# Kernel optimization log

Measured on AMD Instinct MI355X. Metric: run time of the kernel, lower is better.

The kernel has to match this reference:

```python
import jax, jax.numpy as jnp
import numpy as np


def setup_inputs() -> dict:
    T, B, D = 2048, 16, 1024
    key = jax.random.key(0)
    ks = jax.random.split(key, 6)
    scale = 1.0 / np.sqrt(D)  # keep matmul outputs O(1) like xavier/orthogonal init
    return {
        "x": jax.random.normal(ks[0], (T, B, D), dtype=jnp.float32),
        "h0": jnp.zeros((B, D), dtype=jnp.float32),
        "W_alpha": jax.random.normal(ks[1], (D, D), dtype=jnp.float32) * scale,
        "b_alpha": jnp.full((D,), 2.0, dtype=jnp.float32),
        "W_beta": jax.random.normal(ks[2], (D, D), dtype=jnp.float32) * scale,
        "b_beta": jnp.zeros((D,), dtype=jnp.float32),
        "W_h": jax.random.normal(ks[3], (D, D), dtype=jnp.float32) * (0.5 * scale),
        "W_x": jax.random.normal(ks[4], (D, D), dtype=jnp.float32) * scale,
        "b": jnp.zeros((D,), dtype=jnp.float32),
    }


def reference(x, h0, W_alpha, b_alpha, W_beta, b_beta, W_h, W_x, b):
    # x: (T, B, D). Precompute all input-dependent projections as one big GEMM each.
    alpha_all = jax.nn.sigmoid(jnp.einsum("tbd,ed->tbe", x, W_alpha) + b_alpha)  # (T,B,D)
    beta_all = jax.nn.sigmoid(jnp.einsum("tbd,ed->tbe", x, W_beta) + b_beta)
    Wx_all = jnp.einsum("tbd,ed->tbe", x, W_x) + b

    def step(h_prev, inp):
        alpha, beta, wx = inp
        v = jnp.tanh(h_prev @ W_h.T + wx)
        h_new = alpha * h_prev + beta * v
        out = h_new * jax.nn.silu(h_new)
        return h_new, (h_new, out)

    _, (h_seq, output) = jax.lax.scan(step, h0, (alpha_all, beta_all, Wx_all))
    h = jnp.concatenate([h0[None], h_seq], axis=0)  # (T+1, B, D)
    return output, h
```

## Files before the change

### kernel.cpp

```cpp
#include <hip/hip_runtime.h>
#include <stdint.h>
#include <stddef.h>

static constexpr int  T_STEPS   = 2048;
static constexpr int  BATCH     = 16;
static constexpr int  DIM       = 1024;
static constexpr long RROWS     = (long)T_STEPS * BATCH;
static constexpr long BD        = (long)BATCH * DIM;
static constexpr long OUT_ELEMS = (long)T_STEPS * BD;

static constexpr size_t WX_OFF  = 0;
static constexpr size_t XBF_OFF = 134217728;
static constexpr size_t WHI_OFF = XBF_OFF + 67108864;
static constexpr size_t WLO_OFF = WHI_OFF + 6291456;
static constexpr size_t HBP_OFF = WLO_OFF + 6291456;

typedef __attribute__((ext_vector_type(2))) float          f32x2;
typedef __attribute__((ext_vector_type(4))) float          f32x4;
typedef __attribute__((ext_vector_type(8))) short          s16x8;
typedef __attribute__((ext_vector_type(4))) unsigned short u16x4;
typedef __attribute__((ext_vector_type(8))) unsigned short u16x8;

#define AS1 __attribute__((address_space(1)))
#define AS3 __attribute__((address_space(3)))

static __device__ __forceinline__ unsigned short f2bf(float x) {
  union { float f; unsigned u; } a; a.f = x;
  unsigned r = a.u + 0x7fffu + ((a.u >> 16) & 1u);
  return (unsigned short)(r >> 16);
}
static __device__ __forceinline__ float bf2f(unsigned short h) {
  union { unsigned u; float f; } a; a.u = ((unsigned)h) << 16; return a.f;
}
static __device__ __forceinline__ void gload_lds16(const void* g, void* l) {
  __builtin_amdgcn_global_load_lds((const AS1 void*)g, (AS3 void*)l, 16, 0, 0);
}
static __device__ __forceinline__ float fast_tanh(float z) {
  return 1.0f - 2.0f / (__expf(2.0f * z) + 1.0f);
}

__global__ __launch_bounds__(256) void convert_x_kernel(const float* __restrict__ x,
                                                        unsigned short* __restrict__ xbf) {
  const long n8 = (RROWS * DIM) / 8;
  const long stride = (long)gridDim.x * blockDim.x;
  for (long i = (long)blockIdx.x * blockDim.x + threadIdx.x; i < n8; i += stride) {
    const float4* p = (const float4*)(x + i * 8);
    float4 v0 = p[0], v1 = p[1];
    u16x8 o;
    o[0] = f2bf(v0.x); o[1] = f2bf(v0.y); o[2] = f2bf(v0.z); o[3] = f2bf(v0.w);
    o[4] = f2bf(v1.x); o[5] = f2bf(v1.y); o[6] = f2bf(v1.z); o[7] = f2bf(v1.w);
    *(u16x8*)(xbf + i * 8) = o;
  }
}

__global__ __launch_bounds__(256) void convert_w_kernel(const float* __restrict__ Wa,
                                                        const float* __restrict__ Wb,
                                                        const float* __restrict__ Wx,
                                                        unsigned short* __restrict__ whi,
                                                        unsigned short* __restrict__ wlo) {
  const long n4 = (3l * 1024 * 1024) / 4;
  const long stride = (long)gridDim.x * blockDim.x;
  for (long i = (long)blockIdx.x * blockDim.x + threadIdx.x; i < n4; i += stride) {
    long e = i * 4;
    int mat = (int)(e >> 20);
    long off = e & 1048575l;
    const float* src = (mat == 0) ? Wa : (mat == 1) ? Wb : Wx;
    float4 v = *(const float4*)(src + off);
    u16x4 hi, lo;
    hi[0] = f2bf(v.x); lo[0] = f2bf(v.x - bf2f(hi[0]));
    hi[1] = f2bf(v.y); lo[1] = f2bf(v.y - bf2f(hi[1]));
    hi[2] = f2bf(v.z); lo[2] = f2bf(v.z - bf2f(hi[2]));
    hi[3] = f2bf(v.w); lo[3] = f2bf(v.w - bf2f(hi[3]));
    *(u16x4*)(whi + e) = hi;
    *(u16x4*)(wlo + e) = lo;
  }
}

__global__ __launch_bounds__(256) void gemm_pre(
    const unsigned short* __restrict__ xbf,
    const unsigned short* __restrict__ whi,
    const unsigned short* __restrict__ wlo,
    const float* __restrict__ b_alpha, const float* __restrict__ b_beta, const float* __restrict__ b_x,
    float* __restrict__ alpha_dst, float* __restrict__ beta_dst, float* __restrict__ wx_dst)
{
  __shared__ unsigned short Al[128 * 64];
  __shared__ unsigned short Bh[128 * 64];
  __shared__ unsigned short Bl[128 * 64];
  const int tid  = threadIdx.x;
  const int lane = tid & 63;
  const int w    = tid >> 6;
  const int wm   = w >> 1, wn = w & 1;
  const long rowA0 = (long)blockIdx.x * 128;
  const int  colB0 = blockIdx.y * 128;

  f32x4 acc[4][4];
#pragma unroll
  for (int i = 0; i < 4; ++i)
#pragma unroll
    for (int j = 0; j < 4; ++j) acc[i][j] = (f32x4){0.f, 0.f, 0.f, 0.f};

  for (int k0 = 0; k0 < 1024; k0 += 64) {
#pragma unroll
    for (int is = 0; is < 4; ++is) {
      const int o   = is * 4096 + tid * 16;
      const int row = o >> 7;
      const int ke  = (o & 127) >> 1;
      const long asrc = (rowA0 + row) * 1024 + (k0 + ke);
      const long bsrc = ((long)(colB0 + row)) * 1024 + (k0 + ke);
      gload_lds16(xbf + asrc, (char*)Al + is * 4096 + w * 1024);
      gload_lds16(whi + bsrc, (char*)Bh + is * 4096 + w * 1024);
      gload_lds16(wlo + bsrc, (char*)Bl + is * 4096 + w * 1024);
    }
    asm volatile("s_waitcnt vmcnt(0)" ::: "memory");
    __syncthreads();
#pragma unroll
    for (int kk = 0; kk < 2; ++kk) {
      const int koff = kk * 64 + ((lane >> 4) * 16);
      s16x8 a[4], bhf[4], blf[4];
#pragma unroll
      for (int i = 0; i < 4; ++i)
        a[i] = *(const s16x8*)((const char*)Al + (wm * 64 + i * 16 + (lane & 15)) * 128 + koff);
#pragma unroll
      for (int j = 0; j < 4; ++j) {
        const int r = (wn * 64 + j * 16 + (lane & 15)) * 128 + koff;
        bhf[j] = *(const s16x8*)((const char*)Bh + r);
        blf[j] = *(const s16x8*)((const char*)Bl + r);
      }
#pragma unroll
      for (int i = 0; i < 4; ++i)
#pragma unroll
        for (int j = 0; j < 4; ++j) {
          acc[i][j] = __builtin_amdgcn_mfma_f32_16x16x32_bf16(a[i], bhf[j], acc[i][j], 0, 0, 0);
          acc[i][j] = __builtin_amdgcn_mfma_f32_16x16x32_bf16(a[i], blf[j], acc[i][j], 0, 0, 0);
        }
    }
    __syncthreads();
  }

  const int region = colB0 >> 10;
  const float* bias = (region == 0) ? b_alpha : (region == 1) ? b_beta : b_x;
  float* dst = (region == 0) ? alpha_dst : (region == 1) ? beta_dst : wx_dst;
#pragma unroll
  for (int j = 0; j < 4; ++j) {
    const int colg = colB0 + wn * 64 + j * 16 + (lane & 15);
    const int nl = colg & 1023;
    const float bj = bias[nl];
#pragma unroll
    for (int i = 0; i < 4; ++i) {
#pragma unroll
      for (int r = 0; r < 4; ++r) {
        const long rowg = rowA0 + wm * 64 + i * 16 + ((lane >> 4) * 4) + r;
        float z = acc[i][j][r] + bj;
        float val = (region == 2) ? z : (1.0f / (1.0f + __expf(-z)));
        dst[rowg * 1024 + nl] = val;
      }
    }
  }
}

__global__ __launch_bounds__(256, 1) void scan_kernel(
    const float* __restrict__ Wh,
    const float* __restrict__ h0,
    const float* __restrict__ wxb,
    float* __restrict__ out_buf,
    float* __restrict__ h_out,
    unsigned* __restrict__ hbp)
{
  __shared__ unsigned short WhiL[32 * 1024];
  __shared__ unsigned short WloL[32 * 1024];
  __shared__ __align__(16) float zred[2][4][16][34];

  const int tid  = threadIdx.x;
  const int lane = tid & 63;
  const int w    = tid >> 6;
  const int wg   = blockIdx.x;
  const int n0   = wg * 32;

  {
    const int row = tid >> 3;
    const int kb  = (tid & 7) * 128;
    const float* src = Wh + (size_t)(n0 + row) * 1024 + kb;
    const unsigned sx = ((unsigned)(row & 7)) << 4;
    const unsigned rb = (unsigned)row * 2048u;
#pragma unroll
    for (int q = 0; q < 32; ++q) {
      float4 v = *(const float4*)(src + q * 4);
      u16x4 hi, lo;
      hi[0] = f2bf(v.x); lo[0] = f2bf(v.x - bf2f(hi[0]));
      hi[1] = f2bf(v.y); lo[1] = f2bf(v.y - bf2f(hi[1]));
      hi[2] = f2bf(v.z); lo[2] = f2bf(v.z - bf2f(hi[2]));
      hi[3] = f2bf(v.w); lo[3] = f2bf(v.w - bf2f(hi[3]));
      const unsigned addr = (rb + (unsigned)(kb + q * 4) * 2u) ^ sx;
      *(u16x4*)((char*)WhiL + addr) = hi;
      *(u16x4*)((char*)WloL + addr) = lo;
    }
  }

  const int b_own = tid >> 4;
  const int nl    = tid & 15;
  const long off0 = (long)b_own * 1024 + n0 + 2 * nl;
  const int  pword = b_own * 512 + wg * 16 + nl;

  const int arow = lane & 15;
  const int gk   = lane >> 4;
  const unsigned bswz = ((unsigned)(arow & 7)) << 4;

  f32x2 hpv = *(const f32x2*)(h0 + off0);
  float hp0 = hpv[0], hp1 = hpv[1];
  *(f32x2*)(h_out + off0) = hpv;
  {
    unsigned pv = ((unsigned)f2bf(hp1) << 16) | (unsigned)(f2bf(hp0) & 0xFFFEu);
    __hip_atomic_store(hbp + pword, pv, __ATOMIC_RELAXED, __HIP_MEMORY_SCOPE_AGENT);
  }
  __syncthreads();

  f32x2 acv = *(const f32x2*)(h_out + BD + off0);
  f32x2 bcv = *(const f32x2*)(out_buf + off0);
  f32x2 wcv = *(const f32x2*)(wxb + off0);
  float a_c0 = acv[0], a_c1 = acv[1], b_c0 = bcv[0], b_c1 = bcv[1], w_c0 = wcv[0], w_c1 = wcv[1];

  float dh0 = 0.f, dh1 = 0.f;

  for (int t = 0; t < T_STEPS; ++t) {
    const unsigned eps = (unsigned)((t >> 1) & 1);
    const unsigned long long* base64 =
        (const unsigned long long*)hbp +
        (((size_t)(t & 1) * 8192 + (long)arow * 512 + w * 128 + gk * 4) >> 1);

    unsigned long long vv[8][2];
#pragma unroll
    for (int q = 0; q < 8; ++q) {
      vv[q][0] = __hip_atomic_load(base64 + q * 8,     __ATOMIC_RELAXED, __HIP_MEMORY_SCOPE_AGENT);
      vv[q][1] = __hip_atomic_load(base64 + q * 8 + 1, __ATOMIC_RELAXED, __HIP_MEMORY_SCOPE_AGENT);
    }

    float a_n0 = 0.f, a_n1 = 0.f, b_n0 = 0.f, b_n1 = 0.f, w_n0 = 0.f, w_n1 = 0.f;
    if (t + 1 < T_STEPS) {
      const long o = (long)(t + 1) * BD + off0;
      f32x2 an = __builtin_nontemporal_load((const f32x2*)(h_out + BD + o));
      f32x2 bn = __builtin_nontemporal_load((const f32x2*)(out_buf + o));
      f32x2 wn = __builtin_nontemporal_load((const f32x2*)(wxb + o));
      a_n0 = an[0]; a_n1 = an[1]; b_n0 = bn[0]; b_n1 = bn[1]; w_n0 = wn[0]; w_n1 = wn[1];
    }
    __builtin_amdgcn_sched_barrier(0);

    if (t > 0) {
      const long od = (long)(t - 1) * BD + off0;
      f32x2 hv; hv[0] = dh0; hv[1] = dh1;
      __builtin_nontemporal_store(hv, (f32x2*)(h_out + BD + od));
      const float sg0 = 1.0f / (1.0f + __expf(-dh0));
      const float sg1 = 1.0f / (1.0f + __expf(-dh1));
      f32x2 ov; ov[0] = dh0 * dh0 * sg0; ov[1] = dh1 * dh1 * sg1;
      __builtin_nontemporal_store(ov, (f32x2*)(out_buf + od));
    }

    f32x4 acc0 = (f32x4){0.f,0.f,0.f,0.f};
    f32x4 acc1 = (f32x4){0.f,0.f,0.f,0.f};
    const unsigned kbase = (unsigned)(w * 256 + gk * 8) * 2u;
    union Frag { unsigned long long u[2]; s16x8 h; };

#define DO_CHUNK(Q, V)                                                          \
    {                                                                           \
      Frag fh; fh.u[0] = (V)[0]; fh.u[1] = (V)[1];                              \
      const unsigned kb = kbase + (unsigned)(Q) * 64u;                          \
      const unsigned a0 = ((unsigned)arow * 2048u + kb) ^ bswz;                 \
      const unsigned a1 = ((unsigned)(16 + arow) * 2048u + kb) ^ bswz;          \
      s16x8 bh0 = *(const s16x8*)((const char*)WhiL + a0);                      \
      s16x8 bl0 = *(const s16x8*)((const char*)WloL + a0);                      \
      s16x8 bh1 = *(const s16x8*)((const char*)WhiL + a1);                      \
      s16x8 bl1 = *(const s16x8*)((const char*)WloL + a1);                      \
      acc0 = __builtin_amdgcn_mfma_f32_16x16x32_bf16(fh.h, bh0, acc0, 0, 0, 0); \
      acc0 = __builtin_amdgcn_mfma_f32_16x16x32_bf16(fh.h, bl0, acc0, 0, 0, 0); \
      acc1 = __builtin_amdgcn_mfma_f32_16x16x32_bf16(fh.h, bh1, acc1, 0, 0, 0); \
      acc1 = __builtin_amdgcn_mfma_f32_16x16x32_bf16(fh.h, bl1, acc1, 0, 0, 0); \
    }

    unsigned pend = 0;
#pragma unroll
    for (int q = 0; q < 8; ++q) {
      unsigned bad = 0;
#pragma unroll
      for (int d = 0; d < 2; ++d) {
        bad |= ((unsigned)vv[q][d] ^ eps) & 1u;
        bad |= ((unsigned)(vv[q][d] >> 32) ^ eps) & 1u;
      }
      if (__all(bad == 0u)) { DO_CHUNK(q, vv[q]); }
      else                  { pend |= 1u << q; }
    }

    int iters = 0;
    while (pend) {
#pragma unroll
      for (int q = 0; q < 8; ++q)
        if (pend & (1u << q)) {
          vv[q][0] = __hip_atomic_load(base64 + q * 8,     __ATOMIC_RELAXED, __HIP_MEMORY_SCOPE_AGENT);
          vv[q][1] = __hip_atomic_load(base64 + q * 8 + 1, __ATOMIC_RELAXED, __HIP_MEMORY_SCOPE_AGENT);
        }
      __builtin_amdgcn_sched_barrier(0);
#pragma unroll
      for (int q = 0; q < 8; ++q) {
        if (pend & (1u << q)) {
          unsigned bad = 0;
#pragma unroll
          for (int d = 0; d < 2; ++d) {
            bad |= ((unsigned)vv[q][d] ^ eps) & 1u;
            bad |= ((unsigned)(vv[q][d] >> 32) ^ eps) & 1u;
          }
          if (__all(bad == 0u)) { DO_CHUNK(q, vv[q]); pend &= ~(1u << q); }
        }
      }
      if (++iters > (1 << 15)) break;
    }
#undef DO_CHUNK

    const int tb = t & 1;
#pragma unroll
    for (int r = 0; r < 4; ++r) {
      zred[tb][w][gk * 4 + r][arow]      = acc0[r];
      zred[tb][w][gk * 4 + r][16 + arow] = acc1[r];
    }
    __syncthreads();

    float z0 = w_c0, z1 = w_c1;
#pragma unroll
    for (int wv = 0; wv < 4; ++wv) {
      f32x2 p = *(const f32x2*)&zred[tb][wv][b_own][2 * nl];
      z0 += p[0]; z1 += p[1];
    }
    const float v0 = fast_tanh(z0), v1 = fast_tanh(z1);
    const float hn0 = a_c0 * hp0 + b_c0 * v0;
    const float hn1 = a_c1 * hp1 + b_c1 * v1;

    if (t + 1 < T_STEPS) {
      const unsigned epn = (unsigned)(((t + 1) >> 1) & 1);
      unsigned pv = ((unsigned)f2bf(hn1) << 16)
                  | (unsigned)((f2bf(hn0) & 0xFFFEu) | epn);
      __hip_atomic_store(hbp + ((size_t)((t + 1) & 1) * 8192 + pword), pv,
                         __ATOMIC_RELAXED, __HIP_MEMORY_SCOPE_AGENT);
    }

    dh0 = hn0; dh1 = hn1;
    hp0 = hn0; hp1 = hn1;
    a_c0 = a_n0; a_c1 = a_n1; b_c0 = b_n0; b_c1 = b_n1; w_c0 = w_n0; w_c1 = w_n1;
  }

  {
    const long od = (long)(T_STEPS - 1) * BD + off0;
    f32x2 hv; hv[0] = dh0; hv[1] = dh1;
    __builtin_nontemporal_store(hv, (f32x2*)(h_out + BD + od));
    const float sg0 = 1.0f / (1.0f + __expf(-dh0));
    const float sg1 = 1.0f / (1.0f + __expf(-dh1));
    f32x2 ov; ov[0] = dh0 * dh0 * sg0; ov[1] = dh1 * dh1 * sg1;
    __builtin_nontemporal_store(ov, (f32x2*)(out_buf + od));
  }
}

extern "C" void kernel_launch(void* const* d_in, const int* in_sizes, int n_in,
                              void* d_out, int out_size, void* d_ws, size_t ws_size,
                              hipStream_t stream) {
  const float* x  = (const float*)d_in[0];
  const float* h0 = (const float*)d_in[1];
  const float* Wa = (const float*)d_in[2];
  const float* ba = (const float*)d_in[3];
  const float* Wb = (const float*)d_in[4];
  const float* bb = (const float*)d_in[5];
  const float* Wh = (const float*)d_in[6];
  const float* Wx = (const float*)d_in[7];
  const float* bx = (const float*)d_in[8];

  float* out_buf = (float*)d_out;
  float* h_out   = out_buf + OUT_ELEMS;

  char* ws = (char*)d_ws;
  float*          wx_buf = (float*)(ws + WX_OFF);
  unsigned short* xbf    = (unsigned short*)(ws + XBF_OFF);
  unsigned short* whi    = (unsigned short*)(ws + WHI_OFF);
  unsigned short* wlo    = (unsigned short*)(ws + WLO_OFF);
  unsigned*       hbp    = (unsigned*)(ws + HBP_OFF);

  hipMemsetAsync(hbp, 0xFF, 65536, stream);
  convert_x_kernel<<<4096, 256, 0, stream>>>(x, xbf);
  convert_w_kernel<<<1024, 256, 0, stream>>>(Wa, Wb, Wx, whi, wlo);
  gemm_pre<<<dim3(256, 24), 256, 0, stream>>>(xbf, whi, wlo, ba, bb, bx,
                                              h_out + BD, out_buf, wx_buf);
  scan_kernel<<<32, 256, 0, stream>>>(Wh, h0, wx_buf, out_buf, h_out, hbp);
}
```

Before: 8.220 ms.

## Run recurrent scan step on a single wavefront, removing LDS reduction and barrier

The per-step scan work in each block moves from four wavefronts that split K to a single wavefront that walks all 32 K-chunks itself, keeping two accumulator sets per output tile. This removes the per-step shared-memory partial-sum reduction and the __syncthreads between wavefronts, and the epilogue now writes bf16-packed h using lane shuffles. In exchange, one wavefront issues four times as many MFMAs and polling loads per step, with more registers held live and less latency hiding.

```diff
diff --git a/kernel.cpp b/kernel.cpp
--- a/kernel.cpp
+++ b/kernel.cpp
@@ -168,13 +168,10 @@
 {
   __shared__ unsigned short WhiL[32 * 1024];
   __shared__ unsigned short WloL[32 * 1024];
-  __shared__ __align__(16) float zred[2][4][16][34];
-
-  const int tid  = threadIdx.x;
-  const int lane = tid & 63;
-  const int w    = tid >> 6;
-  const int wg   = blockIdx.x;
-  const int n0   = wg * 32;
+
+  const int tid = threadIdx.x;
+  const int wg  = blockIdx.x;
+  const int n0  = wg * 32;
 
   {
     const int row = tid >> 3;
@@ -195,163 +192,202 @@
       *(u16x4*)((char*)WloL + addr) = lo;
     }
   }
-
-  const int b_own = tid >> 4;
-  const int nl    = tid & 15;
-  const long off0 = (long)b_own * 1024 + n0 + 2 * nl;
-  const int  pword = b_own * 512 + wg * 16 + nl;
-
+  __syncthreads();
+  if (tid >= 64) return;
+
+  const int lane = tid;
   const int arow = lane & 15;
   const int gk   = lane >> 4;
   const unsigned bswz = ((unsigned)(arow & 7)) << 4;
 
-  f32x2 hpv = *(const f32x2*)(h0 + off0);
-  float hp0 = hpv[0], hp1 = hpv[1];
-  *(f32x2*)(h_out + off0) = hpv;
-  {
-    unsigned pv = ((unsigned)f2bf(hp1) << 16) | (unsigned)(f2bf(hp0) & 0xFFFEu);
-    __hip_atomic_store(hbp + pword, pv, __ATOMIC_RELAXED, __HIP_MEMORY_SCOPE_AGENT);
-  }
-  __syncthreads();
-
-  f32x2 acv = *(const f32x2*)(h_out + BD + off0);
-  f32x2 bcv = *(const f32x2*)(out_buf + off0);
-  f32x2 wcv = *(const f32x2*)(wxb + off0);
-  float a_c0 = acv[0], a_c1 = acv[1], b_c0 = bcv[0], b_c1 = bcv[1], w_c0 = wcv[0], w_c1 = wcv[1];
-
-  float dh0 = 0.f, dh1 = 0.f;
+  const int gbase = gk * 4096 + n0 + arow;
+  const int jst   = lane & 1;
+  const int pbase = gk * 2048 + (n0 >> 1) + jst * 8 + (arow >> 1);
+
+  float hp[4][2];
+#pragma unroll
+  for (int r = 0; r < 4; ++r)
+#pragma unroll
+    for (int j = 0; j < 2; ++j) {
+      hp[r][j] = h0[gbase + r * 1024 + j * 16];
+      h_out[gbase + r * 1024 + j * 16] = hp[r][j];
+    }
+#pragma unroll
+  for (int r = 0; r < 4; ++r) {
+    unsigned e0 = f2bf(hp[r][0]);
+    unsigned e1 = f2bf(hp[r][1]);
+    unsigned p0 = (unsigned)__shfl_xor((int)e0, 1);
+    unsigned p1 = (unsigned)__shfl_xor((int)e1, 1);
+    unsigned wv = jst ? ((e1 << 16) | (p1 & 0xFFFEu))
+                      : ((p0 << 16) | (e0 & 0xFFFEu));
+    __hip_atomic_store(hbp + pbase + r * 512, wv,
+                       __ATOMIC_RELAXED, __HIP_MEMORY_SCOPE_AGENT);
+  }
+
+  float a_c[4][2], b_c[4][2], w_c[4][2];
+#pragma unroll
+  for (int r = 0; r < 4; ++r)
+#pragma unroll
+    for (int j = 0; j < 2; ++j) {
+      const int o = gbase + r * 1024 + j * 16;
+      a_c[r][j] = h_out[BD + o];
+      b_c[r][j] = out_buf[o];
+      w_c[r][j] = wxb[o];
+    }
+
+  float dh[4][2];
+#pragma unroll
+  for (int r = 0; r < 4; ++r) { dh[r][0] = 0.f; dh[r][1] = 0.f; }
 
   for (int t = 0; t < T_STEPS; ++t) {
     const unsigned eps = (unsigned)((t >> 1) & 1);
     const unsigned long long* base64 =
-        (const unsigned long long*)hbp +
-        (((size_t)(t & 1) * 8192 + (long)arow * 512 + w * 128 + gk * 4) >> 1);
-
-    unsigned long long vv[8][2];
-#pragma unroll
-    for (int q = 0; q < 8; ++q) {
-      vv[q][0] = __hip_atomic_load(base64 + q * 8,     __ATOMIC_RELAXED, __HIP_MEMORY_SCOPE_AGENT);
-      vv[q][1] = __hip_atomic_load(base64 + q * 8 + 1, __ATOMIC_RELAXED, __HIP_MEMORY_SCOPE_AGENT);
-    }
-
-    float a_n0 = 0.f, a_n1 = 0.f, b_n0 = 0.f, b_n1 = 0.f, w_n0 = 0.f, w_n1 = 0.f;
+        (const unsigned long long*)hbp + (size_t)(t & 1) * 4096 + arow * 256 + gk * 2;
+
+    unsigned long long vv[32][2];
+#pragma unroll
+    for (int c = 0; c < 32; ++c) {
+      vv[c][0] = __hip_atomic_load(base64 + c * 8,     __ATOMIC_RELAXED, __HIP_MEMORY_SCOPE_AGENT);
+      vv[c][1] = __hip_atomic_load(base64 + c * 8 + 1, __ATOMIC_RELAXED, __HIP_MEMORY_SCOPE_AGENT);
+    }
+
+    float a_n[4][2], b_n[4][2], w_n[4][2];
     if (t + 1 < T_STEPS) {
-      const long o = (long)(t + 1) * BD + off0;
-      f32x2 an = __builtin_nontemporal_load((const f32x2*)(h_out + BD + o));
-      f32x2 bn = __builtin_nontemporal_load((const f32x2*)(out_buf + o));
-      f32x2 wn = __builtin_nontemporal_load((const f32x2*)(wxb + o));
-      a_n0 = an[0]; a_n1 = an[1]; b_n0 = bn[0]; b_n1 = bn[1]; w_n0 = wn[0]; w_n1 = wn[1];
+      const long o = (long)(t + 1) * BD + gbase;
+#pragma unroll
+      for (int r = 0; r < 4; ++r)
+#pragma unroll
+        for (int j = 0; j < 2; ++j) {
+          const long oo = o + r * 1024 + j * 16;
+          a_n[r][j] = __builtin_nontemporal_load(h_out + BD + oo);
+          b_n[r][j] = __builtin_nontemporal_load(out_buf + oo);
+          w_n[r][j] = __builtin_nontemporal_load(wxb + oo);
+        }
+    } else {
+#pragma unroll
+      for (int r = 0; r < 4; ++r)
+#pragma unroll
+        for (int j = 0; j < 2; ++j) { a_n[r][j] = 0.f; b_n[r][j] = 0.f; w_n[r][j] = 0.f; }
     }
     __builtin_amdgcn_sched_barrier(0);
 
     if (t > 0) {
-      const long od = (long)(t - 1) * BD + off0;
-      f32x2 hv; hv[0] = dh0; hv[1] = dh1;
-      __builtin_nontemporal_store(hv, (f32x2*)(h_out + BD + od));
-      const float sg0 = 1.0f / (1.0f + __expf(-dh0));
-      const float sg1 = 1.0f / (1.0f + __expf(-dh1));
-      f32x2 ov; ov[0] = dh0 * dh0 * sg0; ov[1] = dh1 * dh1 * sg1;
-      __builtin_nontemporal_store(ov, (f32x2*)(out_buf + od));
-    }
-
-    f32x4 acc0 = (f32x4){0.f,0.f,0.f,0.f};
-    f32x4 acc1 = (f32x4){0.f,0.f,0.f,0.f};
-    const unsigned kbase = (unsigned)(w * 256 + gk * 8) * 2u;
+      const long od = (long)(t - 1) * BD + gbase;
+#pragma unroll
+      for (int r = 0; r < 4; ++r)
+#pragma unroll
+        for (int j = 0; j < 2; ++j) {
+          const long oo = od + r * 1024 + j * 16;
+          const float d = dh[r][j];
+          __builtin_nontemporal_store(d, h_out + BD + oo);
+          const float sg = 1.0f / (1.0f + __expf(-d));
+          __builtin_nontemporal_store(d * d * sg, out_buf + oo);
+        }
+    }
+
+    f32x4 ac[2][2];
+    ac[0][0] = (f32x4){0.f,0.f,0.f,0.f}; ac[0][1] = (f32x4){0.f,0.f,0.f,0.f};
+    ac[1][0] = (f32x4){0.f,0.f,0.f,0.f}; ac[1][1] = (f32x4){0.f,0.f,0.f,0.f};
     union Frag { unsigned long long u[2]; s16x8 h; };
 
-#define DO_CHUNK(Q, V)                                                          \
-    {                                                                           \
-      Frag fh; fh.u[0] = (V)[0]; fh.u[1] = (V)[1];                              \
-      const unsigned kb = kbase + (unsigned)(Q) * 64u;                          \
-      const unsigned a0 = ((unsigned)arow * 2048u + kb) ^ bswz;                 \
-      const unsigned a1 = ((unsigned)(16 + arow) * 2048u + kb) ^ bswz;          \
-      s16x8 bh0 = *(const s16x8*)((const char*)WhiL + a0);                      \
-      s16x8 bl0 = *(const s16x8*)((const char*)WloL + a0);                      \
-      s16x8 bh1 = *(const s16x8*)((const char*)WhiL + a1);                      \
-      s16x8 bl1 = *(const s16x8*)((const char*)WloL + a1);                      \
-      acc0 = __builtin_amdgcn_mfma_f32_16x16x32_bf16(fh.h, bh0, acc0, 0, 0, 0); \
-      acc0 = __builtin_amdgcn_mfma_f32_16x16x32_bf16(fh.h, bl0, acc0, 0, 0, 0); \
-      acc1 = __builtin_amdgcn_mfma_f32_16x16x32_bf16(fh.h, bh1, acc1, 0, 0, 0); \
-      acc1 = __builtin_amdgcn_mfma_f32_16x16x32_bf16(fh.h, bl1, acc1, 0, 0, 0); \
+#define DO_CHUNK(C, V)                                                            \
+    {                                                                             \
+      Frag fh; fh.u[0] = (V)[0]; fh.u[1] = (V)[1];                                \
+      const unsigned kb = (unsigned)(C) * 64u + (unsigned)gk * 16u;               \
+      const unsigned a0 = ((unsigned)arow * 2048u + kb) ^ bswz;                   \
+      const unsigned a1 = ((unsigned)(16 + arow) * 2048u + kb) ^ bswz;            \
+      s16x8 bh0 = *(const s16x8*)((const char*)WhiL + a0);                        \
+      s16x8 bl0 = *(const s16x8*)((const char*)WloL + a0);                        \
+      s16x8 bh1 = *(const s16x8*)((const char*)WhiL + a1);                        \
+      s16x8 bl1 = *(const s16x8*)((const char*)WloL + a1);                        \
+      ac[0][(C) & 1] = __builtin_amdgcn_mfma_f32_16x16x32_bf16(fh.h, bh0, ac[0][(C) & 1], 0, 0, 0); \
+      ac[0][(C) & 1] = __builtin_amdgcn_mfma_f32_16x16x32_bf16(fh.h, bl0, ac[0][(C) & 1], 0, 0, 0); \
+      ac[1][(C) & 1] = __builtin_amdgcn_mfma_f32_16x16x32_bf16(fh.h, bh1, ac[1][(C) & 1], 0, 0, 0); \
+      ac[1][(C) & 1] = __builtin_amdgcn_mfma_f32_16x16x32_bf16(fh.h, bl1, ac[1][(C) & 1], 0, 0, 0); \
     }
 
     unsigned pend = 0;
 #pragma unroll
-    for (int q = 0; q < 8; ++q) {
-      unsigned bad = 0;
-#pragma unroll
-      for (int d = 0; d < 2; ++d) {
-        bad |= ((unsigned)vv[q][d] ^ eps) & 1u;
-        bad |= ((unsigned)(vv[q][d] >> 32) ^ eps) & 1u;
-      }
-      if (__all(bad == 0u)) { DO_CHUNK(q, vv[q]); }
-      else                  { pend |= 1u << q; }
+    for (int c = 0; c < 32; ++c) {
+      unsigned bad = ((unsigned)vv[c][0] ^ eps) & 1u;
+      bad |= ((unsigned)(vv[c][0] >> 32) ^ eps) & 1u;
+      bad |= ((unsigned)vv[c][1] ^ eps) & 1u;
+      bad |= ((unsigned)(vv[c][1] >> 32) ^ eps) & 1u;
+      if (__all(bad == 0u)) { DO_CHUNK(c, vv[c]); }
+      else                  { pend |= 1u << c; }
     }
 
     int iters = 0;
     while (pend) {
 #pragma unroll
-      for (int q = 0; q < 8; ++q)
-        if (pend & (1u << q)) {
-          vv[q][0] = __hip_atomic_load(base64 + q * 8,     __ATOMIC_RELAXED, __HIP_MEMORY_SCOPE_AGENT);
-          vv[q][1] = __hip_atomic_load(base64 + q * 8 + 1, __ATOMIC_RELAXED, __HIP_MEMORY_SCOPE_AGENT);
+      for (int c = 0; c < 32; ++c)
+        if (pend & (1u << c)) {
+          vv[c][0] = __hip_atomic_load(base64 + c * 8,     __ATOMIC_RELAXED, __HIP_MEMORY_SCOPE_AGENT);
+          vv[c][1] = __hip_atomic_load(base64 + c * 8 + 1, __ATOMIC_RELAXED, __HIP_MEMORY_SCOPE_AGENT);
         }
       __builtin_amdgcn_sched_barrier(0);
 #pragma unroll
-      for (int q = 0; q < 8; ++q) {
-        if (pend & (1u << q)) {
-          unsigned bad = 0;
-#pragma unroll
-          for (int d = 0; d < 2; ++d) {
-            bad |= ((unsigned)vv[q][d] ^ eps) & 1u;
-            bad |= ((unsigned)(vv[q][d] >> 32) ^ eps) & 1u;
-          }
-          if (__all(bad == 0u)) { DO_CHUNK(q, vv[q]); pend &= ~(1u << q); }
+      for (int c = 0; c < 32; ++c) {
+        if (pend & (1u << c)) {
+          unsigned bad = ((unsigned)vv[c][0] ^ eps) & 1u;
+          bad |= ((unsigned)(vv[c][0] >> 32) ^ eps) & 1u;
+          bad |= ((unsigned)vv[c][1] ^ eps) & 1u;
+          bad |= ((unsigned)(vv[c][1] >> 32) ^ eps) & 1u;
+          if (__all(bad == 0u)) { DO_CHUNK(c, vv[c]); pend &= ~(1u << c); }
         }
       }
       if (++iters > (1 << 15)) break;
     }
 #undef DO_CHUNK
 
-    const int tb = t & 1;
+    const f32x4 zj0 = ac[0][0] + ac[0][1];
+    const f32x4 zj1 = ac[1][0] + ac[1][1];
+    float hn[4][2];
 #pragma unroll
     for (int r = 0; r < 4; ++r) {
-      zred[tb][w][gk * 4 + r][arow]      = acc0[r];
-      zred[tb][w][gk * 4 + r][16 + arow] = acc1[r];
-    }
-    __syncthreads();
-
-    float z0 = w_c0, z1 = w_c1;
-#pragma unroll
-    for (int wv = 0; wv < 4; ++wv) {
-      f32x2 p = *(const f32x2*)&zred[tb][wv][b_own][2 * nl];
-      z0 += p[0]; z1 += p[1];
-    }
-    const float v0 = fast_tanh(z0), v1 = fast_tanh(z1);
-    const float hn0 = a_c0 * hp0 + b_c0 * v0;
-    const float hn1 = a_c1 * hp1 + b_c1 * v1;
+      const float z0 = zj0[r] + w_c[r][0];
+      const float z1 = zj1[r] + w_c[r][1];
+      hn[r][0] = a_c[r][0] * hp[r][0] + b_c[r][0] * fast_tanh(z0);
+      hn[r][1] = a_c[r][1] * hp[r][1] + b_c[r][1] * fast_tanh(z1);
+    }
 
     if (t + 1 < T_STEPS) {
       const unsigned epn = (unsigned)(((t + 1) >> 1) & 1);
-      unsigned pv = ((unsigned)f2bf(hn1) << 16)
-                  | (unsigned)((f2bf(hn0) & 0xFFFEu) | epn);
-      __hip_atomic_store(hbp + ((size_t)((t + 1) & 1) * 8192 + pword), pv,
-                         __ATOMIC_RELAXED, __HIP_MEMORY_SCOPE_AGENT);
-    }
-
-    dh0 = hn0; dh1 = hn1;
-    hp0 = hn0; hp1 = hn1;
-    a_c0 = a_n0; a_c1 = a_n1; b_c0 = b_n0; b_c1 = b_n1; w_c0 = w_n0; w_c1 = w_n1;
+      unsigned* dst = hbp + (size_t)((t + 1) & 1) * 8192 + pbase;
+#pragma unroll
+      for (int r = 0; r < 4; ++r) {
+        unsigned e0 = f2bf(hn[r][0]);
+        unsigned e1 = f2bf(hn[r][1]);
+        unsigned p0 = (unsigned)__shfl_xor((int)e0, 1);
+        unsigned p1 = (unsigned)__shfl_xor((int)e1, 1);
+        unsigned wv = jst ? ((e1 << 16) | ((p1 & 0xFFFEu) | epn))
+                          : ((p0 << 16) | ((e0 & 0xFFFEu) | epn));
+        __hip_atomic_store(dst + r * 512, wv,
+                           __ATOMIC_RELAXED, __HIP_MEMORY_SCOPE_AGENT);
+      }
+    }
+
+#pragma unroll
+    for (int r = 0; r < 4; ++r)
+#pragma unroll
+      for (int j = 0; j < 2; ++j) {
+        dh[r][j] = hn[r][j]; hp[r][j] = hn[r][j];
+        a_c[r][j] = a_n[r][j]; b_c[r][j] = b_n[r][j]; w_c[r][j] = w_n[r][j];
+      }
   }
 
   {
-    const long od = (long)(T_STEPS - 1) * BD + off0;
-    f32x2 hv; hv[0] = dh0; hv[1] = dh1;
-    __builtin_nontemporal_store(hv, (f32x2*)(h_out + BD + od));
-    const float sg0 = 1.0f / (1.0f + __expf(-dh0));
-    const float sg1 = 1.0f / (1.0f + __expf(-dh1));
-    f32x2 ov; ov[0] = dh0 * dh0 * sg0; ov[1] = dh1 * dh1 * sg1;
-    __builtin_nontemporal_store(ov, (f32x2*)(out_buf + od));
+    const long od = (long)(T_STEPS - 1) * BD + gbase;
+#pragma unroll
+    for (int r = 0; r < 4; ++r)
+#pragma unroll
+      for (int j = 0; j < 2; ++j) {
+        const long oo = od + r * 1024 + j * 16;
+        const float d = dh[r][j];
+        __builtin_nontemporal_store(d, h_out + BD + oo);
+        const float sg = 1.0f / (1.0f + __expf(-d));
+        __builtin_nontemporal_store(d * d * sg, out_buf + oo);
+      }
   }
 }
 
```

New measurement: 20.51 ms. +149.6%, slower.
